# Optimization experiments

Measured on AMD Instinct MI355X. Metric: run time of the kernel, lower is better.

Reference implementation:

```python
import jax, jax.numpy as jnp
import numpy as np

# Module hyperparameters (from init_kwargs)
HID = 2048          # hidden_dim
LAT = 512           # kv_latent_dim
H = 16              # num_heads
D = HID // H        # head_dim = 128
FORGET_P = 0.1      # forget_prob
WIN = 128           # window_size
SINK = 16           # persistent_tokens
B, S = 2, 2048
NEG = -1e9


def setup_inputs() -> dict:
    key = jax.random.key(0)
    ks = jax.random.split(key, 8)
    scale = 0.02
    x = jax.random.normal(ks[0], (B, S, HID), dtype=jnp.float32)
    W_q = jax.random.normal(ks[1], (HID, HID), dtype=jnp.float32) * scale
    W_dkv = jax.random.normal(ks[2], (HID, LAT), dtype=jnp.float32) * scale
    W_uk = jax.random.normal(ks[3], (LAT, HID), dtype=jnp.float32) * scale
    W_uv = jax.random.normal(ks[4], (LAT, HID), dtype=jnp.float32) * scale
    W_o = jax.random.normal(ks[5], (HID, HID), dtype=jnp.float32) * scale
    # Bernoulli(forget_prob) per-key forget mask (1 = forget this token)
    forget_mask = jax.random.bernoulli(ks[6], FORGET_P, (B, S)).astype(jnp.int32)
    return {"x": x, "W_q": W_q, "W_dkv": W_dkv, "W_uk": W_uk,
            "W_uv": W_uv, "W_o": W_o, "forget_mask": forget_mask, "top_k": 64}


def reference(x, W_q, W_dkv, W_uk, W_uv, W_o, forget_mask, top_k):
    Bx, Sx, _ = x.shape
    # Queries; keys/values via shared compressed KV latent (MLA-style)
    q = (x @ W_q).reshape(Bx, Sx, H, D)
    c = x @ W_dkv                                   # [B, S, LAT]
    k = (c @ W_uk).reshape(Bx, Sx, H, D)
    v = (c @ W_uv).reshape(Bx, Sx, H, D)

    scores = jnp.einsum('bqhd,bkhd->bhqk', q, k) / np.float32(np.sqrt(D))

    qi = jnp.arange(Sx)[:, None]
    ki = jnp.arange(Sx)[None, :]
    causal = ki <= qi
    local = ki >= qi - (WIN - 1)
    sink = ki < SINK                  # persistent sink tokens always visible
    allow = causal & (local | sink)   # [S, S]

    # Forgetting: drop non-sink, non-self keys flagged by the forget mask
    forget = (forget_mask[:, None, None, :] == 1) \
             & (ki >= SINK)[None, None] & (ki != qi)[None, None]   # [B,1,S,S]
    keep = allow[None, None] & ~forget

    s = jnp.where(keep, scores, jnp.asarray(NEG, scores.dtype))
    # Top-k selection per query: keep only the k largest scores
    kth = jax.lax.top_k(s, top_k)[0][..., -1:]
    s = jnp.where(s >= kth, s, jnp.asarray(NEG, s.dtype))

    attn = jax.nn.softmax(s, axis=-1)
    out = jnp.einsum('bhqk,bkhd->bqhd', attn, v).reshape(Bx, Sx, HID)
    return out @ W_o
```

## Files before the change

### kernel.cpp

```cpp
#include <hip/hip_runtime.h>
#include <hip/hip_bf16.h>

typedef unsigned short u16;
typedef unsigned int u32;
typedef unsigned long long u64;
typedef __bf16 bf16x8 __attribute__((ext_vector_type(8)));
typedef float f32x4 __attribute__((ext_vector_type(4)));
typedef u16 u16x4 __attribute__((ext_vector_type(4)));
typedef u16 u16x8 __attribute__((ext_vector_type(8)));

static constexpr int BB = 2, SS = 2048, HIDC = 2048, LATC = 512, NH = 16, HD = 128;
static constexpr int MROWS = BB * SS;
static constexpr float NEGV = -1e9f;

__device__ __forceinline__ u16 f2bf(float f) {
  __hip_bfloat16 h = __float2bfloat16(f);
  return __builtin_bit_cast(u16, h);
}
__device__ __forceinline__ float bf2f(u16 u) {
  return __uint_as_float(((u32)u) << 16);
}
__device__ __forceinline__ void load_lds16(const void* g, void* l) {
  __builtin_amdgcn_global_load_lds(
      (const __attribute__((address_space(1))) void*)g,
      (__attribute__((address_space(3))) void*)l, 16, 0, 0);
}

template <int MODE>
__global__ __launch_bounds__(256, 2) void gemm_bt(
    const u16* __restrict__ A, const u16* __restrict__ Bt,
    float* __restrict__ C, u16* __restrict__ Cb, int M, int N, int K) {
  __shared__ u16 As[128 * 64];
  __shared__ u16 Bs[128 * 64];
  const int tid = threadIdx.x;
  const int lane = tid & 63;
  const int wv = tid >> 6;
  const int wr = wv >> 1, wc = wv & 1;
  const int m0 = blockIdx.x * 128, n0 = blockIdx.y * 128;

  f32x4 acc[4][4];
#pragma unroll
  for (int i = 0; i < 4; ++i)
#pragma unroll
    for (int j = 0; j < 4; ++j) acc[i][j] = (f32x4){0.f, 0.f, 0.f, 0.f};

  int srow[4], sgc[4];
#pragma unroll
  for (int j = 0; j < 4; ++j) {
    int e = j * 2048 + tid * 8;
    int row = e >> 6;
    int slot = (e >> 3) & 7;
    srow[j] = row;
    sgc[j] = (slot ^ (row & 7)) * 8;
  }

  for (int k0 = 0; k0 < K; k0 += 64) {
    __syncthreads();
#pragma unroll
    for (int j = 0; j < 4; ++j) {
      const u16* ga = A + (size_t)(m0 + srow[j]) * K + k0 + sgc[j];
      const u16* gb = Bt + (size_t)(n0 + srow[j]) * K + k0 + sgc[j];
      load_lds16(ga, &As[j * 2048 + wv * 512]);
      load_lds16(gb, &Bs[j * 2048 + wv * 512]);
    }
    asm volatile("s_waitcnt vmcnt(0)" ::: "memory");
    __syncthreads();

#pragma unroll
    for (int kk = 0; kk < 2; ++kk) {
      bf16x8 afr[4], bfr[4];
      const int kg = kk * 4 + (lane >> 4);
#pragma unroll
      for (int i = 0; i < 4; ++i) {
        int ar = wr * 64 + i * 16 + (lane & 15);
        afr[i] = *(const bf16x8*)&As[ar * 64 + ((kg ^ (ar & 7)) << 3)];
        int br = wc * 64 + i * 16 + (lane & 15);
        bfr[i] = *(const bf16x8*)&Bs[br * 64 + ((kg ^ (br & 7)) << 3)];
      }
#pragma unroll
      for (int mi = 0; mi < 4; ++mi)
#pragma unroll
        for (int ni = 0; ni < 4; ++ni)
          acc[mi][ni] = __builtin_amdgcn_mfma_f32_16x16x32_bf16(
              afr[mi], bfr[ni], acc[mi][ni], 0, 0, 0);
    }
  }

#pragma unroll
  for (int mi = 0; mi < 4; ++mi) {
#pragma unroll
    for (int ni = 0; ni < 4; ++ni) {
      const int row = m0 + wr * 64 + mi * 16 + (lane >> 4) * 4;
      const int col = n0 + wc * 64 + ni * 16 + (lane & 15);
#pragma unroll
      for (int r = 0; r < 4; ++r) {
        size_t off = (size_t)(row + r) * N + col;
        if constexpr (MODE == 0) C[off] = acc[mi][ni][r];
        if constexpr (MODE == 2) Cb[off] = f2bf(acc[mi][ni][r]);
      }
    }
  }
}

template <int TN, int MODE>
__global__ __launch_bounds__(256, 2) void gemm_split_bt(
    const u16* __restrict__ Ah, const u16* __restrict__ Al,
    const u16* __restrict__ Bth, const u16* __restrict__ Btl,
    float* __restrict__ C, u16* __restrict__ Ch, u16* __restrict__ Cl,
    int M, int N, int K) {
  constexpr int NI = TN / 32;
  __shared__ u16 Ash[128 * 64];
  __shared__ u16 Asl[128 * 64];
  __shared__ u16 Bsh[TN * 64];
  __shared__ u16 Bsl[TN * 64];
  const int tid = threadIdx.x;
  const int lane = tid & 63;
  const int wv = tid >> 6;
  const int wr = wv >> 1, wc = wv & 1;
  const int l15 = lane & 15, lhi = lane >> 4;
  const int m0 = blockIdx.x * 128, n0 = blockIdx.y * TN;

  f32x4 acc[4][NI];
#pragma unroll
  for (int i = 0; i < 4; ++i)
#pragma unroll
    for (int j = 0; j < NI; ++j) acc[i][j] = (f32x4){0.f, 0.f, 0.f, 0.f};

  int srow[4], sgc[4];
#pragma unroll
  for (int j = 0; j < 4; ++j) {
    int e = j * 2048 + tid * 8;
    int row = e >> 6;
    int slot = (e >> 3) & 7;
    srow[j] = row;
    sgc[j] = (slot ^ (row & 7)) * 8;
  }

  for (int k0 = 0; k0 < K; k0 += 64) {
    __syncthreads();
#pragma unroll
    for (int j = 0; j < 4; ++j) {
      const size_t ao = (size_t)(m0 + srow[j]) * K + k0 + sgc[j];
      load_lds16(Ah + ao, &Ash[j * 2048 + wv * 512]);
      load_lds16(Al + ao, &Asl[j * 2048 + wv * 512]);
    }
#pragma unroll
    for (int j = 0; j < NI; ++j) {
      const size_t bo = (size_t)(n0 + srow[j]) * K + k0 + sgc[j];
      load_lds16(Bth + bo, &Bsh[j * 2048 + wv * 512]);
      load_lds16(Btl + bo, &Bsl[j * 2048 + wv * 512]);
    }
    asm volatile("s_waitcnt vmcnt(0)" ::: "memory");
    __syncthreads();

#pragma unroll
    for (int kk = 0; kk < 2; ++kk) {
      const int kg = kk * 4 + lhi;
      bf16x8 afh[4], afl[4], bfh[NI], bfl[NI];
#pragma unroll
      for (int i = 0; i < 4; ++i) {
        const int ar = wr * 64 + i * 16 + l15;
        const int off = ar * 64 + ((kg ^ (ar & 7)) << 3);
        afh[i] = *(const bf16x8*)&Ash[off];
        afl[i] = *(const bf16x8*)&Asl[off];
      }
#pragma unroll
      for (int i = 0; i < NI; ++i) {
        const int br = wc * (TN / 2) + i * 16 + l15;
        const int off = br * 64 + ((kg ^ (br & 7)) << 3);
        bfh[i] = *(const bf16x8*)&Bsh[off];
        bfl[i] = *(const bf16x8*)&Bsl[off];
      }
#pragma unroll
      for (int mi = 0; mi < 4; ++mi)
#pragma unroll
        for (int ni = 0; ni < NI; ++ni) {
          acc[mi][ni] = __builtin_amdgcn_mfma_f32_16x16x32_bf16(
              afh[mi], bfh[ni], acc[mi][ni], 0, 0, 0);
          acc[mi][ni] = __builtin_amdgcn_mfma_f32_16x16x32_bf16(
              afh[mi], bfl[ni], acc[mi][ni], 0, 0, 0);
          acc[mi][ni] = __builtin_amdgcn_mfma_f32_16x16x32_bf16(
              afl[mi], bfh[ni], acc[mi][ni], 0, 0, 0);
        }
    }
  }

#pragma unroll
  for (int mi = 0; mi < 4; ++mi) {
#pragma unroll
    for (int ni = 0; ni < NI; ++ni) {
      const int row = m0 + wr * 64 + mi * 16 + lhi * 4;
      const int col = n0 + wc * (TN / 2) + ni * 16 + l15;
#pragma unroll
      for (int r = 0; r < 4; ++r) {
        const size_t off = (size_t)(row + r) * N + col;
        const float v = acc[mi][ni][r];
        if constexpr (MODE == 0) C[off] = v;
        if constexpr (MODE == 3) {
          const u16 hh = f2bf(v);
          Ch[off] = hh;
          Cl[off] = f2bf(v - bf2f(hh));
        }
      }
    }
  }
}

__global__ __launch_bounds__(1024) void transpose_split(
    const float* __restrict__ W, u16* __restrict__ Th, u16* __restrict__ Tl,
    int K, int N) {
  __shared__ float t[32][33];
  const int tx = threadIdx.x, ty = threadIdx.y;
  t[ty][tx] = W[(size_t)(blockIdx.y * 32 + ty) * N + blockIdx.x * 32 + tx];
  __syncthreads();
  const float v = t[tx][ty];
  const u16 hi = f2bf(v);
  const u16 lo = f2bf(v - bf2f(hi));
  const size_t o = (size_t)(blockIdx.x * 32 + ty) * K + blockIdx.y * 32 + tx;
  Th[o] = hi;
  Tl[o] = lo;
}

__global__ __launch_bounds__(1024) void transpose_one(
    const float* __restrict__ W, u16* __restrict__ T, int K, int N) {
  __shared__ float t[32][33];
  const int tx = threadIdx.x, ty = threadIdx.y;
  t[ty][tx] = W[(size_t)(blockIdx.y * 32 + ty) * N + blockIdx.x * 32 + tx];
  __syncthreads();
  const size_t o = (size_t)(blockIdx.x * 32 + ty) * K + blockIdx.y * 32 + tx;
  T[o] = f2bf(t[tx][ty]);
}

__global__ void split_ew(const float* __restrict__ in, u16* __restrict__ hi,
                         u16* __restrict__ lo, int n) {
  const size_t i = ((size_t)blockIdx.x * blockDim.x + threadIdx.x) * 4;
  if (i >= (size_t)n) return;
  f32x4 v = *(const f32x4*)(in + i);
  u16x4 h, l;
#pragma unroll
  for (int e = 0; e < 4; ++e) {
    float f = v[e];
    u16 hh = f2bf(f);
    h[e] = hh;
    l[e] = f2bf(f - bf2f(hh));
  }
  *(u16x4*)(hi + i) = h;
  *(u16x4*)(lo + i) = l;
}

__device__ __forceinline__ u32 fmap(float f) {
  u32 b = __float_as_uint(f);
  return (b & 0x80000000u) ? ~b : (b | 0x80000000u);
}
__device__ __forceinline__ float unfmap(u32 u) {
  return (u & 0x80000000u) ? __uint_as_float(u ^ 0x80000000u)
                           : __uint_as_float(~u);
}

__global__ __launch_bounds__(256, 3) void attn_v4(
    const u16* __restrict__ qbh, const u16* __restrict__ qbl,
    const u16* __restrict__ khi, const u16* __restrict__ klo,
    const u16* __restrict__ vt, const int* __restrict__ forget,
    const int* __restrict__ topk, u16* __restrict__ ab) {
  __shared__ u16 KP[2 * 64 * 128];
  __shared__ float St[64 * 68];
  __shared__ int fm[256];
  u16* const Kh = KP;
  u16* const Kl = KP + 64 * 128;
  u16* const Pb = KP;
  u16* const Vts = (u16*)St;

  const float scale = 0.08838834764831845f;
  const int tid = threadIdx.x, lane = tid & 63, wv = tid >> 6;
  const int q0 = blockIdx.x * 64;
  const int h = blockIdx.y, b = blockIdx.z;
  const int l15 = lane & 15, lhi = lane >> 4;
  const int nt = (q0 >= 256) ? 4 : (q0 / 64 + 1);
  const int KTOP = topk[0];

  auto kbase = [&](int t) {
    return (q0 >= 256) ? (t == 0 ? 0 : q0 + t * 64 - 192) : t * 64;
  };
  auto stage_k = [&](int t) {
    const int kbt = kbase(t);
#pragma unroll
    for (int p = 0; p < 4; ++p) {
      const int c = p * 256 + tid;
      const int row = c >> 4, sl = c & 15;
      const size_t src = (size_t)(b * SS + kbt + row) * HIDC + h * HD +
                         ((sl ^ (row & 7)) << 3);
      load_lds16(khi + src, Kh + (p * 256 + wv * 64) * 8);
      load_lds16(klo + src, Kl + (p * 256 + wv * 64) * 8);
    }
  };
  auto stage_vt = [&](int t) {
    const int kbt = kbase(t);
#pragma unroll
    for (int p = 0; p < 4; ++p) {
      const int c = p * 256 + tid;
      const int d = c >> 3, sl = c & 7;
      const u16* src = vt + ((size_t)(b * HIDC + h * HD + d)) * SS + kbt +
                       ((sl ^ (d & 7)) << 3);
      load_lds16(src, Vts + (p * 256 + wv * 64) * 8);
    }
  };

  fm[tid] = ((tid >> 6) < nt) ? forget[b * SS + kbase(tid >> 6) + (tid & 63)] : 0;

  u16x8 ah[4], al[4];
  const size_t qrow = (size_t)(b * SS + q0 + wv * 16 + l15) * HIDC + h * HD;
#pragma unroll
  for (int kt = 0; kt < 4; ++kt) {
    ah[kt] = *(const u16x8*)(qbh + qrow + kt * 32 + lhi * 8);
    al[kt] = *(const u16x8*)(qbl + qrow + kt * 32 + lhi * 8);
  }

  u32 uu[16][4];
#pragma unroll
  for (int i = 0; i < 16; ++i)
#pragma unroll
    for (int j = 0; j < 4; ++j) uu[i][j] = 0u;

  stage_k(0);
#pragma unroll
  for (int t = 0; t < 4; ++t) {
    if (t < nt) {
      asm volatile("s_waitcnt vmcnt(0)" ::: "memory");
      __syncthreads();

      f32x4 acc[4];
#pragma unroll
      for (int ni = 0; ni < 4; ++ni) acc[ni] = (f32x4){0.f, 0.f, 0.f, 0.f};
#pragma unroll
      for (int kt = 0; kt < 4; ++kt) {
        const int kg = kt * 4 + lhi;
#pragma unroll
        for (int ni = 0; ni < 4; ++ni) {
          const int key = ni * 16 + l15;
          const int off = key * 128 + ((kg ^ (key & 7)) << 3);
          const bf16x8 bh = *(const bf16x8*)(Kh + off);
          const bf16x8 bl = *(const bf16x8*)(Kl + off);
          acc[ni] = __builtin_amdgcn_mfma_f32_16x16x32_bf16(
              __builtin_bit_cast(bf16x8, ah[kt]), bh, acc[ni], 0, 0, 0);
          acc[ni] = __builtin_amdgcn_mfma_f32_16x16x32_bf16(
              __builtin_bit_cast(bf16x8, ah[kt]), bl, acc[ni], 0, 0, 0);
          acc[ni] = __builtin_amdgcn_mfma_f32_16x16x32_bf16(
              __builtin_bit_cast(bf16x8, al[kt]), bh, acc[ni], 0, 0, 0);
        }
      }
#pragma unroll
      for (int ni = 0; ni < 4; ++ni)
#pragma unroll
        for (int r = 0; r < 4; ++r)
          St[(wv * 16 + lhi * 4 + r) * 68 + ni * 16 + l15] = acc[ni][r] * scale;
      __syncthreads();

      if (t + 1 < nt) stage_k(t + 1);

      const int kbt = kbase(t);
#pragma unroll
      for (int i = 0; i < 16; ++i) {
        const int qi = q0 + wv * 16 + i;
        const int key = kbt + lane;
        const bool valid =
            key <= qi && (key >= qi - 127 || key < 16) &&
            !(fm[t * 64 + lane] && key >= 16 && key != qi);
        uu[i][t] = fmap(valid ? St[(wv * 16 + i) * 68 + lane] : NEGV);
      }
    }
  }
  __syncthreads();

  stage_vt(0);

  u32 tl[16], th[16];
#pragma unroll
  for (int i = 0; i < 16; ++i) { tl[i] = 0u; th[i] = 0xFFFFFFFFu; }
  for (int it = 0; it < 32; ++it) {
#pragma unroll
    for (int i = 0; i < 16; ++i) {
      const u32 mid = tl[i] + ((th[i] - tl[i]) >> 1) + 1u;
      const int cnt = __popcll(__ballot(uu[i][0] >= mid)) +
                      __popcll(__ballot(uu[i][1] >= mid)) +
                      __popcll(__ballot(uu[i][2] >= mid)) +
                      __popcll(__ballot(uu[i][3] >= mid));
      const bool ge = cnt >= KTOP;
      tl[i] = ge ? mid : tl[i];
      th[i] = ge ? th[i] : mid - 1u;
    }
  }

#pragma unroll
  for (int i = 0; i < 16; ++i) {
    const int r = wv * 16 + i;
    float sv[4], m = NEGV;
#pragma unroll
    for (int j = 0; j < 4; ++j) {
      sv[j] = unfmap(uu[i][j]);
      m = (uu[i][j] >= tl[i]) ? fmaxf(m, sv[j]) : m;
    }
#pragma unroll
    for (int off = 32; off > 0; off >>= 1) m = fmaxf(m, __shfl_xor(m, off));
    float e[4], z = 0.f;
#pragma unroll
    for (int j = 0; j < 4; ++j) {
      e[j] = (uu[i][j] >= tl[i]) ? __expf(sv[j] - m) : 0.f;
      z += e[j];
    }
#pragma unroll
    for (int off = 32; off > 0; off >>= 1) z += __shfl_xor(z, off);
    const float rz = 1.f / z;
#pragma unroll
    for (int j = 0; j < 4; ++j) {
      const int c = lane + 64 * j;
      const int sl = c >> 3;
      Pb[r * 256 + ((sl ^ (r & 7)) << 3) + (c & 7)] = f2bf(e[j] * rz);
    }
  }

  asm volatile("s_waitcnt vmcnt(0)" ::: "memory");
  __syncthreads();

  f32x4 pacc[8];
#pragma unroll
  for (int t2 = 0; t2 < 8; ++t2) pacc[t2] = (f32x4){0.f, 0.f, 0.f, 0.f};

#pragma unroll
  for (int t = 0; t < 4; ++t) {
    if (t < nt) {
#pragma unroll
      for (int ks = 0; ks < 2; ++ks) {
        const int arow = wv * 16 + l15;
        const int aslot = t * 8 + ks * 4 + lhi;
        const bf16x8 af =
            *(const bf16x8*)(Pb + arow * 256 + ((aslot ^ (arow & 7)) << 3));
#pragma unroll
        for (int t2 = 0; t2 < 8; ++t2) {
          const int drow = t2 * 16 + l15;
          const int dslot = ks * 4 + lhi;
          const bf16x8 bf_ =
              *(const bf16x8*)(Vts + drow * 64 + ((dslot ^ (drow & 7)) << 3));
          pacc[t2] = __builtin_amdgcn_mfma_f32_16x16x32_bf16(af, bf_, pacc[t2],
                                                             0, 0, 0);
        }
      }
      if (t + 1 < nt) {
        __syncthreads();
        stage_vt(t + 1);
        asm volatile("s_waitcnt vmcnt(0)" ::: "memory");
        __syncthreads();
      }
    }
  }

#pragma unroll
  for (int t2 = 0; t2 < 8; ++t2)
#pragma unroll
    for (int r = 0; r < 4; ++r) {
      const int row = q0 + wv * 16 + lhi * 4 + r;
      const int col = h * HD + t2 * 16 + l15;
      ab[(size_t)(b * SS + row) * HIDC + col] = f2bf(pacc[t2][r]);
    }
}

extern "C" void kernel_launch(void* const* d_in, const int* in_sizes, int n_in,
                              void* d_out, int out_size, void* d_ws, size_t ws_size,
                              hipStream_t stream) {
  const float* x = (const float*)d_in[0];
  const float* W_q = (const float*)d_in[1];
  const float* W_dkv = (const float*)d_in[2];
  const float* W_uk = (const float*)d_in[3];
  const float* W_uv = (const float*)d_in[4];
  const float* W_o = (const float*)d_in[5];
  const int* forget = (const int*)d_in[6];
  const int* topk = (const int*)d_in[7];
  float* out = (float*)d_out;

  char* p = (char*)d_ws;
  auto take = [&](size_t n) {
    char* r = p;
    p += (n + 255) & ~(size_t)255;
    return r;
  };

  u16* xb_hi = (u16*)take((size_t)MROWS * HIDC * 2);
  u16* xb_lo = (u16*)take((size_t)MROWS * HIDC * 2);
  u16* Wqh = (u16*)take((size_t)HIDC * HIDC * 2);
  u16* Wql = (u16*)take((size_t)HIDC * HIDC * 2);
  u16* Wdh = (u16*)take((size_t)LATC * HIDC * 2);
  u16* Wdl = (u16*)take((size_t)LATC * HIDC * 2);
  u16* Wukh = (u16*)take((size_t)HIDC * LATC * 2);
  u16* Wukl = (u16*)take((size_t)HIDC * LATC * 2);
  u16* Wuvt = (u16*)take((size_t)HIDC * LATC * 2);
  u16* Wot = (u16*)take((size_t)HIDC * HIDC * 2);
  u16* qbh = (u16*)take((size_t)MROWS * HIDC * 2);
  u16* qbl = (u16*)take((size_t)MROWS * HIDC * 2);
  u16* cbh = (u16*)take((size_t)MROWS * LATC * 2);
  u16* cbl = (u16*)take((size_t)MROWS * LATC * 2);
  u16* vt = (u16*)take((size_t)BB * HIDC * SS * 2);
  u16* khi = xb_hi;
  u16* klo = xb_lo;
  u16* ab = Wqh;

  const dim3 tb(32, 32);
  split_ew<<<dim3((MROWS * HIDC / 4) / 256), dim3(256), 0, stream>>>(
      x, xb_hi, xb_lo, MROWS * HIDC);
  transpose_split<<<dim3(HIDC / 32, HIDC / 32), tb, 0, stream>>>(W_q, Wqh, Wql, HIDC, HIDC);
  transpose_split<<<dim3(LATC / 32, HIDC / 32), tb, 0, stream>>>(W_dkv, Wdh, Wdl, HIDC, LATC);
  transpose_split<<<dim3(HIDC / 32, LATC / 32), tb, 0, stream>>>(W_uk, Wukh, Wukl, LATC, HIDC);
  transpose_one<<<dim3(HIDC / 32, LATC / 32), tb, 0, stream>>>(W_uv, Wuvt, LATC, HIDC);
  transpose_one<<<dim3(HIDC / 32, HIDC / 32), tb, 0, stream>>>(W_o, Wot, HIDC, HIDC);

  gemm_split_bt<128, 3><<<dim3(MROWS / 128, HIDC / 128), 256, 0, stream>>>(
      xb_hi, xb_lo, Wqh, Wql, nullptr, qbh, qbl, MROWS, HIDC, HIDC);
  gemm_split_bt<64, 3><<<dim3(MROWS / 128, LATC / 64), 256, 0, stream>>>(
      xb_hi, xb_lo, Wdh, Wdl, nullptr, cbh, cbl, MROWS, LATC, HIDC);
  gemm_split_bt<128, 3><<<dim3(MROWS / 128, HIDC / 128), 256, 0, stream>>>(
      cbh, cbl, Wukh, Wukl, nullptr, khi, klo, MROWS, HIDC, LATC);
  const dim3 gv(HIDC / 128, SS / 128);
  gemm_bt<2><<<gv, 256, 0, stream>>>(Wuvt, cbh, nullptr, vt, HIDC, SS, LATC);
  gemm_bt<2><<<gv, 256, 0, stream>>>(Wuvt, cbh + (size_t)SS * LATC, nullptr,
                                     vt + (size_t)HIDC * SS, HIDC, SS, LATC);
  attn_v4<<<dim3(SS / 64, NH, BB), dim3(256), 0, stream>>>(
      qbh, qbl, khi, klo, vt, forget, topk, ab);
  gemm_bt<0><<<dim3(MROWS / 128, HIDC / 128), 256, 0, stream>>>(
      ab, Wot, out, nullptr, MROWS, HIDC, HIDC);
}
```

Measured before the change: 369.7 us.

## Use 512-thread attention blocks with split key/dim work and double-buffered V

The attention kernel doubles its block to 8 waves. Each pair of waves splits the QK^T key columns and the PV output dimensions, and each wave now handles 8 query rows for the top-k bisection and softmax instead of 16. A second LDS buffer for V^T lets the next V tile load while the current one is multiplied, which removes one barrier per tile. The aim is to cut per-wave register pressure and serial top-k work and to hide V load latency, at the cost of more LDS per block and lower occupancy per block (launch bounds 512,2).

```diff
diff --git a/kernel.cpp b/kernel.cpp
--- a/kernel.cpp
+++ b/kernel.cpp
@@ -257,23 +257,25 @@
                            : __uint_as_float(~u);
 }
 
-__global__ __launch_bounds__(256, 3) void attn_v4(
+__global__ __launch_bounds__(512, 2) void attn_v5(
     const u16* __restrict__ qbh, const u16* __restrict__ qbl,
     const u16* __restrict__ khi, const u16* __restrict__ klo,
     const u16* __restrict__ vt, const int* __restrict__ forget,
     const int* __restrict__ topk, u16* __restrict__ ab) {
   __shared__ u16 KP[2 * 64 * 128];
   __shared__ float St[64 * 68];
+  __shared__ u16 Vb1[64 * 128];
   __shared__ int fm[256];
   u16* const Kh = KP;
   u16* const Kl = KP + 64 * 128;
   u16* const Pb = KP;
-  u16* const Vts = (u16*)St;
+  u16* const Vt0 = (u16*)St;
 
   const float scale = 0.08838834764831845f;
   const int tid = threadIdx.x, lane = tid & 63, wv = tid >> 6;
   const int q0 = blockIdx.x * 64;
   const int h = blockIdx.y, b = blockIdx.z;
+  const int mt = wv >> 1, nh = wv & 1;
   const int l15 = lane & 15, lhi = lane >> 4;
   const int nt = (q0 >= 256) ? 4 : (q0 / 64 + 1);
   const int KTOP = topk[0];
@@ -284,40 +286,41 @@
   auto stage_k = [&](int t) {
     const int kbt = kbase(t);
 #pragma unroll
-    for (int p = 0; p < 4; ++p) {
-      const int c = p * 256 + tid;
+    for (int p = 0; p < 2; ++p) {
+      const int c = p * 512 + tid;
       const int row = c >> 4, sl = c & 15;
       const size_t src = (size_t)(b * SS + kbt + row) * HIDC + h * HD +
                          ((sl ^ (row & 7)) << 3);
-      load_lds16(khi + src, Kh + (p * 256 + wv * 64) * 8);
-      load_lds16(klo + src, Kl + (p * 256 + wv * 64) * 8);
+      load_lds16(khi + src, Kh + (p * 512 + wv * 64) * 8);
+      load_lds16(klo + src, Kl + (p * 512 + wv * 64) * 8);
     }
   };
-  auto stage_vt = [&](int t) {
+  auto stage_vt = [&](int t, u16* dst) {
     const int kbt = kbase(t);
 #pragma unroll
-    for (int p = 0; p < 4; ++p) {
-      const int c = p * 256 + tid;
+    for (int p = 0; p < 2; ++p) {
+      const int c = p * 512 + tid;
       const int d = c >> 3, sl = c & 7;
       const u16* src = vt + ((size_t)(b * HIDC + h * HD + d)) * SS + kbt +
                        ((sl ^ (d & 7)) << 3);
-      load_lds16(src, Vts + (p * 256 + wv * 64) * 8);
+      load_lds16(src, dst + (p * 512 + wv * 64) * 8);
     }
   };
 
-  fm[tid] = ((tid >> 6) < nt) ? forget[b * SS + kbase(tid >> 6) + (tid & 63)] : 0;
+  if (tid < 256)
+    fm[tid] = ((tid >> 6) < nt) ? forget[b * SS + kbase(tid >> 6) + (tid & 63)] : 0;
 
   u16x8 ah[4], al[4];
-  const size_t qrow = (size_t)(b * SS + q0 + wv * 16 + l15) * HIDC + h * HD;
+  const size_t qrow = (size_t)(b * SS + q0 + mt * 16 + l15) * HIDC + h * HD;
 #pragma unroll
   for (int kt = 0; kt < 4; ++kt) {
     ah[kt] = *(const u16x8*)(qbh + qrow + kt * 32 + lhi * 8);
     al[kt] = *(const u16x8*)(qbl + qrow + kt * 32 + lhi * 8);
   }
 
-  u32 uu[16][4];
-#pragma unroll
-  for (int i = 0; i < 16; ++i)
+  u32 uu[8][4];
+#pragma unroll
+  for (int i = 0; i < 8; ++i)
 #pragma unroll
     for (int j = 0; j < 4; ++j) uu[i][j] = 0u;
 
@@ -328,57 +331,59 @@
       asm volatile("s_waitcnt vmcnt(0)" ::: "memory");
       __syncthreads();
 
-      f32x4 acc[4];
-#pragma unroll
-      for (int ni = 0; ni < 4; ++ni) acc[ni] = (f32x4){0.f, 0.f, 0.f, 0.f};
+      f32x4 acc0 = (f32x4){0.f, 0.f, 0.f, 0.f};
+      f32x4 acc1 = (f32x4){0.f, 0.f, 0.f, 0.f};
 #pragma unroll
       for (int kt = 0; kt < 4; ++kt) {
         const int kg = kt * 4 + lhi;
 #pragma unroll
-        for (int ni = 0; ni < 4; ++ni) {
-          const int key = ni * 16 + l15;
+        for (int ni = 0; ni < 2; ++ni) {
+          const int key = nh * 32 + ni * 16 + l15;
           const int off = key * 128 + ((kg ^ (key & 7)) << 3);
           const bf16x8 bh = *(const bf16x8*)(Kh + off);
           const bf16x8 bl = *(const bf16x8*)(Kl + off);
-          acc[ni] = __builtin_amdgcn_mfma_f32_16x16x32_bf16(
-              __builtin_bit_cast(bf16x8, ah[kt]), bh, acc[ni], 0, 0, 0);
-          acc[ni] = __builtin_amdgcn_mfma_f32_16x16x32_bf16(
-              __builtin_bit_cast(bf16x8, ah[kt]), bl, acc[ni], 0, 0, 0);
-          acc[ni] = __builtin_amdgcn_mfma_f32_16x16x32_bf16(
-              __builtin_bit_cast(bf16x8, al[kt]), bh, acc[ni], 0, 0, 0);
+          f32x4 a = ni ? acc1 : acc0;
+          a = __builtin_amdgcn_mfma_f32_16x16x32_bf16(
+              __builtin_bit_cast(bf16x8, ah[kt]), bh, a, 0, 0, 0);
+          a = __builtin_amdgcn_mfma_f32_16x16x32_bf16(
+              __builtin_bit_cast(bf16x8, ah[kt]), bl, a, 0, 0, 0);
+          a = __builtin_amdgcn_mfma_f32_16x16x32_bf16(
+              __builtin_bit_cast(bf16x8, al[kt]), bh, a, 0, 0, 0);
+          if (ni) acc1 = a; else acc0 = a;
         }
       }
 #pragma unroll
-      for (int ni = 0; ni < 4; ++ni)
+      for (int ni = 0; ni < 2; ++ni)
 #pragma unroll
         for (int r = 0; r < 4; ++r)
-          St[(wv * 16 + lhi * 4 + r) * 68 + ni * 16 + l15] = acc[ni][r] * scale;
+          St[(mt * 16 + lhi * 4 + r) * 68 + nh * 32 + ni * 16 + l15] =
+              (ni ? acc1 : acc0)[r] * scale;
       __syncthreads();
 
       if (t + 1 < nt) stage_k(t + 1);
 
       const int kbt = kbase(t);
 #pragma unroll
-      for (int i = 0; i < 16; ++i) {
-        const int qi = q0 + wv * 16 + i;
+      for (int i = 0; i < 8; ++i) {
+        const int qi = q0 + wv * 8 + i;
         const int key = kbt + lane;
         const bool valid =
             key <= qi && (key >= qi - 127 || key < 16) &&
             !(fm[t * 64 + lane] && key >= 16 && key != qi);
-        uu[i][t] = fmap(valid ? St[(wv * 16 + i) * 68 + lane] : NEGV);
+        uu[i][t] = fmap(valid ? St[(wv * 8 + i) * 68 + lane] : NEGV);
       }
     }
   }
   __syncthreads();
 
-  stage_vt(0);
-
-  u32 tl[16], th[16];
-#pragma unroll
-  for (int i = 0; i < 16; ++i) { tl[i] = 0u; th[i] = 0xFFFFFFFFu; }
+  stage_vt(0, Vt0);
+
+  u32 tl[8], th[8];
+#pragma unroll
+  for (int i = 0; i < 8; ++i) { tl[i] = 0u; th[i] = 0xFFFFFFFFu; }
   for (int it = 0; it < 32; ++it) {
 #pragma unroll
-    for (int i = 0; i < 16; ++i) {
+    for (int i = 0; i < 8; ++i) {
       const u32 mid = tl[i] + ((th[i] - tl[i]) >> 1) + 1u;
       const int cnt = __popcll(__ballot(uu[i][0] >= mid)) +
                       __popcll(__ballot(uu[i][1] >= mid)) +
@@ -391,8 +396,8 @@
   }
 
 #pragma unroll
-  for (int i = 0; i < 16; ++i) {
-    const int r = wv * 16 + i;
+  for (int i = 0; i < 8; ++i) {
+    const int r = wv * 8 + i;
     float sv[4], m = NEGV;
 #pragma unroll
     for (int j = 0; j < 4; ++j) {
@@ -421,32 +426,32 @@
   asm volatile("s_waitcnt vmcnt(0)" ::: "memory");
   __syncthreads();
 
-  f32x4 pacc[8];
-#pragma unroll
-  for (int t2 = 0; t2 < 8; ++t2) pacc[t2] = (f32x4){0.f, 0.f, 0.f, 0.f};
+  f32x4 pacc[4];
+#pragma unroll
+  for (int t2 = 0; t2 < 4; ++t2) pacc[t2] = (f32x4){0.f, 0.f, 0.f, 0.f};
 
 #pragma unroll
   for (int t = 0; t < 4; ++t) {
     if (t < nt) {
+      if (t + 1 < nt) stage_vt(t + 1, ((t + 1) & 1) ? Vb1 : Vt0);
+      const u16* Vcur = (t & 1) ? Vb1 : Vt0;
 #pragma unroll
       for (int ks = 0; ks < 2; ++ks) {
-        const int arow = wv * 16 + l15;
+        const int arow = mt * 16 + l15;
         const int aslot = t * 8 + ks * 4 + lhi;
         const bf16x8 af =
             *(const bf16x8*)(Pb + arow * 256 + ((aslot ^ (arow & 7)) << 3));
 #pragma unroll
-        for (int t2 = 0; t2 < 8; ++t2) {
-          const int drow = t2 * 16 + l15;
+        for (int t2 = 0; t2 < 4; ++t2) {
+          const int drow = nh * 64 + t2 * 16 + l15;
           const int dslot = ks * 4 + lhi;
           const bf16x8 bf_ =
-              *(const bf16x8*)(Vts + drow * 64 + ((dslot ^ (drow & 7)) << 3));
+              *(const bf16x8*)(Vcur + drow * 64 + ((dslot ^ (drow & 7)) << 3));
           pacc[t2] = __builtin_amdgcn_mfma_f32_16x16x32_bf16(af, bf_, pacc[t2],
                                                              0, 0, 0);
         }
       }
       if (t + 1 < nt) {
-        __syncthreads();
-        stage_vt(t + 1);
         asm volatile("s_waitcnt vmcnt(0)" ::: "memory");
         __syncthreads();
       }
@@ -454,11 +459,11 @@
   }
 
 #pragma unroll
-  for (int t2 = 0; t2 < 8; ++t2)
+  for (int t2 = 0; t2 < 4; ++t2)
 #pragma unroll
     for (int r = 0; r < 4; ++r) {
-      const int row = q0 + wv * 16 + lhi * 4 + r;
-      const int col = h * HD + t2 * 16 + l15;
+      const int row = q0 + mt * 16 + lhi * 4 + r;
+      const int col = h * HD + nh * 64 + t2 * 16 + l15;
       ab[(size_t)(b * SS + row) * HIDC + col] = f2bf(pacc[t2][r]);
     }
 }
@@ -521,7 +526,7 @@
   gemm_bt<2><<<gv, 256, 0, stream>>>(Wuvt, cbh, nullptr, vt, HIDC, SS, LATC);
   gemm_bt<2><<<gv, 256, 0, stream>>>(Wuvt, cbh + (size_t)SS * LATC, nullptr,
                                      vt + (size_t)HIDC * SS, HIDC, SS, LATC);
-  attn_v4<<<dim3(SS / 64, NH, BB), dim3(256), 0, stream>>>(
+  attn_v5<<<dim3(SS / 64, NH, BB), dim3(512), 0, stream>>>(
       qbh, qbl, khi, klo, vt, forget, topk, ab);
   gemm_bt<0><<<dim3(MROWS / 128, HIDC / 128), 256, 0, stream>>>(
       ab, Wot, out, nullptr, MROWS, HIDC, HIDC);
```

After: 349.4 us. 1.06x faster.
